# Optimization experiments

Measured on AMD Instinct MI355X. Metric: run time of the kernel, lower is better.

## Reference

```python
import jax, jax.numpy as jnp
import numpy as np

N = 20000            # nodes
E = 320000           # edges (before self loops)
NUM_PLAYERS = 5000
FEAT = 64            # feature_dim
H = 128              # hidden_dim
OUT = 10             # out_features
NEG_SLOPE = 0.2


def _p(key, shape, fan_in):
    return jax.random.normal(key, shape, dtype=jnp.float32) / np.sqrt(fan_in)


def setup_inputs() -> dict:
    key = jax.random.key(0)
    ks = jax.random.split(key, 20)
    # x_player: col 0 = player id (stored as float), cols 1: = features
    ids = jax.random.randint(ks[0], (N, 1), 0, NUM_PLAYERS + 1).astype(jnp.float32)
    feats = jax.random.normal(ks[1], (N, FEAT), dtype=jnp.float32)
    x_player = jnp.concatenate([ids, feats], axis=1)
    edge_index = jax.random.randint(ks[2], (2, E), 0, N, dtype=jnp.int32)
    return {
        "x_player": x_player,
        "edge_index": edge_index,
        "emb": jax.random.normal(ks[3], (NUM_PLAYERS + 1, H), dtype=jnp.float32),
        "proj_W": _p(ks[4], (H + FEAT, H), H + FEAT),
        "proj_b": jnp.zeros((H,), jnp.float32),
        "W1l": _p(ks[5], (H, 4 * H), H),
        "W1r": _p(ks[6], (H, 4 * H), H),
        "att1": _p(ks[7], (4, H), H),
        "b1": jnp.zeros((4 * H,), jnp.float32),
        "W2l": _p(ks[8], (4 * H, H), 4 * H),
        "W2r": _p(ks[9], (4 * H, H), 4 * H),
        "att2": _p(ks[10], (1, H), H),
        "b2": jnp.zeros((H,), jnp.float32),
        "out_W": _p(ks[11], (H, OUT), H),
        "out_b": jnp.zeros((OUT,), jnp.float32),
    }


def gatv2(x, src, dst, Wl, Wr, att, bias, heads, ch, concat):
    # GATv2Conv (PyG defaults: share_weights=False, negative_slope=0.2,
    # add_self_loops handled by caller, dropout off at eval)
    xl = (x @ Wl).reshape(N, heads, ch)   # source transform (x_j)
    xr = (x @ Wr).reshape(N, heads, ch)   # target transform (x_i)
    h = xl[src] + xr[dst]                                      # [E,H,C]
    e = jnp.sum(jax.nn.leaky_relu(h, NEG_SLOPE) * att, -1)     # [E,H]
    # segment softmax over incoming edges of each dst node
    m = jax.ops.segment_max(e, dst, num_segments=N)            # [N,H]
    ex = jnp.exp(e - m[dst])
    s = jax.ops.segment_sum(ex, dst, num_segments=N)
    alpha = ex / (s[dst] + 1e-16)                              # [E,H]
    out = jax.ops.segment_sum(alpha[..., None] * xl[src], dst, num_segments=N)
    out = out.reshape(N, heads * ch) if concat else out.mean(axis=1)
    return out + bias


def reference(x_player, edge_index, emb, proj_W, proj_b,
              W1l, W1r, att1, b1, W2l, W2r, att2, b2, out_W, out_b):
    ids = x_player[:, 0].astype(jnp.int32)
    combined = jnp.concatenate([emb[ids], x_player[:, 1:]], axis=1)
    x = jax.nn.relu(combined @ proj_W + proj_b)                # [N,H]
    # add self loops (GATv2Conv default)
    loop = jnp.arange(N, dtype=edge_index.dtype)
    src = jnp.concatenate([edge_index[0], loop])
    dst = jnp.concatenate([edge_index[1], loop])
    x = jax.nn.relu(gatv2(x, src, dst, W1l, W1r, att1, b1, 4, H, True))
    x = gatv2(x, src, dst, W2l, W2r, att2, b2, 1, H, True)
    return x @ out_W + out_b                                   # [N,OUT]
```

## Files before the change

kernel.cpp:

```cpp
#include <hip/hip_runtime.h>
#include <math.h>

#define NNODES 20000
#define XP_COLS 65

typedef unsigned int uint32;
typedef __attribute__((ext_vector_type(8))) short short8;
typedef __attribute__((ext_vector_type(4))) float float4v;

__device__ __forceinline__ float bflo(uint32 u){ return __uint_as_float(u << 16); }
__device__ __forceinline__ float bfhi(uint32 u){ return __uint_as_float(u & 0xffff0000u); }
__device__ __forceinline__ unsigned short f2bf(float f){
  uint32 u = __float_as_uint(f);
  uint32 r = (u + 0x7fffu + ((u >> 16) & 1u)) >> 16;
  return (unsigned short)r;
}
__device__ __forceinline__ void unpack8(uint4 u, float* x){
  x[0]=bflo(u.x); x[1]=bfhi(u.x); x[2]=bflo(u.y); x[3]=bfhi(u.y);
  x[4]=bflo(u.z); x[5]=bfhi(u.z); x[6]=bflo(u.w); x[7]=bfhi(u.w);
}

__global__ void k_count(const int* __restrict__ dst, int E, int* __restrict__ deg){
  int e = blockIdx.x * 256 + threadIdx.x;
  if (e < E) atomicAdd(&deg[dst[e]], 1);
}

__global__ __launch_bounds__(256) void k_scan(const int* __restrict__ deg,
                                              int* __restrict__ off,
                                              int* __restrict__ cursor){
  const int CH = 80;
  int tid = threadIdx.x;
  int lane = tid & 63, w = tid >> 6;
  int beg = tid * CH;
  bool act = beg < NNODES;
  int sum = 0;
  if (act){
    const int4* p = (const int4*)(deg + beg);
    #pragma unroll
    for (int i = 0; i < 20; i++){
      int4 v = p[i];
      sum += v.x + v.y + v.z + v.w + 4;
    }
  }
  int inc = sum;
  #pragma unroll
  for (int d = 1; d < 64; d <<= 1){
    int t = __shfl_up(inc, d, 64);
    if (lane >= d) inc += t;
  }
  __shared__ int wtot[4];
  if (lane == 63) wtot[w] = inc;
  __syncthreads();
  int wbase = 0;
  for (int i = 0; i < w; i++) wbase += wtot[i];
  int run = wbase + inc - sum;
  if (act){
    const int4* p = (const int4*)(deg + beg);
    int4* po = (int4*)(off + beg);
    int4* pc = (int4*)(cursor + beg);
    #pragma unroll
    for (int i = 0; i < 20; i++){
      int4 v = p[i];
      int4 o;
      o.x = run; run += v.x + 1;
      o.y = run; run += v.y + 1;
      o.z = run; run += v.z + 1;
      o.w = run; run += v.w + 1;
      po[i] = o; pc[i] = o;
    }
  }
  if (tid == 249) off[NNODES] = run;
}

__global__ void k_fill(const int* __restrict__ src, const int* __restrict__ dst, int E,
                       int* __restrict__ cursor, int* __restrict__ csr){
  int t = blockIdx.x * 256 + threadIdx.x;
  if (t < NNODES){
    int p = atomicAdd(&cursor[t], 1);
    csr[p] = t;
  } else if (t < NNODES + E){
    int e = t - NNODES;
    int p = atomicAdd(&cursor[dst[e]], 1);
    csr[p] = src[e];
  }
}

__global__ void k_cvt(const float* __restrict__ W1l, const float* __restrict__ W1r,
                      const float* __restrict__ W2l, const float* __restrict__ W2r,
                      const float* __restrict__ projW,
                      unsigned short* __restrict__ T1l, unsigned short* __restrict__ T1r,
                      unsigned short* __restrict__ T2l, unsigned short* __restrict__ T2r,
                      unsigned short* __restrict__ Tp){
  int idx = blockIdx.x * 256 + threadIdx.x;
  if (idx < 65536){
    int o = idx;
    int n = o >> 7, k = o & 127;
    T1l[o] = f2bf(W1l[k * 512 + n]);
  } else if (idx < 131072){
    int o = idx - 65536;
    int n = o >> 7, k = o & 127;
    T1r[o] = f2bf(W1r[k * 512 + n]);
  } else if (idx < 196608){
    int o = idx - 131072;
    int n = o >> 9, k = o & 511;
    T2l[o] = f2bf(W2l[k * 128 + n]);
  } else if (idx < 262144){
    int o = idx - 196608;
    int n = o >> 9, k = o & 511;
    T2r[o] = f2bf(W2r[k * 128 + n]);
  } else if (idx < 286720){
    int o = idx - 262144;
    int n = o / 192, k = o - n * 192;
    Tp[o] = f2bf(projW[k * 128 + n]);
  }
}

__global__ __launch_bounds__(256) void k_proj_mfma(const float* __restrict__ xp,
                                                   const float* __restrict__ emb,
                                                   const unsigned short* __restrict__ Bt,
                                                   const float* __restrict__ bias,
                                                   unsigned short* __restrict__ Xb){
  __shared__ unsigned short As[64][40];
  __shared__ unsigned short Bs[128][40];
  __shared__ int ids[64];
  int tid = threadIdx.x;
  int bm = blockIdx.x * 64;
  int w = tid >> 6, lane = tid & 63;
  int wm = (w >> 1) * 32, wn = (w & 1) * 64;
  int quad = lane >> 4, l16 = lane & 15;
  if (tid < 64){
    int g = bm + tid;
    ids[tid] = (g < NNODES) ? (int)xp[(size_t)g * XP_COLS] : 0;
  }
  float4v acc[2][4];
  #pragma unroll
  for (int i = 0; i < 2; i++)
    #pragma unroll
    for (int j = 0; j < 4; j++) acc[i][j] = (float4v){0.f,0.f,0.f,0.f};
  int am = tid >> 2, ak = (tid & 3) * 8;
  int gm = bm + am;
  bool mv = gm < NNODES;
  int brow = tid >> 1, bk = (tid & 1) * 16;
  __syncthreads();

  for (int k0 = 0; k0 < 192; k0 += 32){
    float v[8];
    if (k0 < 128){
      const float* ep = emb + (size_t)ids[am] * 128 + k0 + ak;
      float4 e0 = *(const float4*)ep;
      float4 e1 = *(const float4*)(ep + 4);
      v[0]=e0.x; v[1]=e0.y; v[2]=e0.z; v[3]=e0.w;
      v[4]=e1.x; v[5]=e1.y; v[6]=e1.z; v[7]=e1.w;
    } else {
      const float* fp = xp + (size_t)gm * XP_COLS + 1 + (k0 - 128) + ak;
      #pragma unroll
      for (int i = 0; i < 8; i++) v[i] = mv ? fp[i] : 0.f;
    }
    ushort4 o0, o1;
    o0.x=f2bf(v[0]); o0.y=f2bf(v[1]); o0.z=f2bf(v[2]); o0.w=f2bf(v[3]);
    o1.x=f2bf(v[4]); o1.y=f2bf(v[5]); o1.z=f2bf(v[6]); o1.w=f2bf(v[7]);
    *(ushort4*)&As[am][ak]     = o0;
    *(ushort4*)&As[am][ak + 4] = o1;
    const unsigned short* bp = Bt + (size_t)brow * 192 + k0 + bk;
    *(uint4*)&Bs[brow][bk]     = *(const uint4*)bp;
    *(uint4*)&Bs[brow][bk + 8] = *(const uint4*)(bp + 8);
    __syncthreads();
    short8 af[2], bf[4];
    #pragma unroll
    for (int t = 0; t < 2; t++) af[t] = *(const short8*)&As[wm + t * 16 + l16][quad * 8];
    #pragma unroll
    for (int t = 0; t < 4; t++) bf[t] = *(const short8*)&Bs[wn + t * 16 + l16][quad * 8];
    #pragma unroll
    for (int tm = 0; tm < 2; tm++)
      #pragma unroll
      for (int tn = 0; tn < 4; tn++)
        acc[tm][tn] = __builtin_amdgcn_mfma_f32_16x16x32_bf16(af[tm], bf[tn], acc[tm][tn], 0, 0, 0);
    __syncthreads();
  }
  #pragma unroll
  for (int tm = 0; tm < 2; tm++){
    #pragma unroll
    for (int r = 0; r < 4; r++){
      int row = bm + wm + tm * 16 + quad * 4 + r;
      if (row >= NNODES) continue;
      #pragma unroll
      for (int tn = 0; tn < 4; tn++){
        int col = wn + tn * 16 + l16;
        float val = fmaxf(acc[tm][tn][r] + bias[col], 0.f);
        Xb[(size_t)row * 128 + col] = f2bf(val);
      }
    }
  }
}

template<int K, int N, int MODE, int NH>
__global__ __launch_bounds__(256) void k_mfma(const unsigned short* __restrict__ A,
                                              const unsigned short* __restrict__ B0t,
                                              const unsigned short* __restrict__ B1t,
                                              void* __restrict__ C0, void* __restrict__ C1,
                                              const float* __restrict__ att,
                                              float* __restrict__ dl, float* __restrict__ dr){
  const unsigned short* Bt = blockIdx.z ? B1t : B0t;
  __shared__ unsigned short As[64][40];
  __shared__ unsigned short Bs[128][40];
  __shared__ float red[4][32];
  int tid = threadIdx.x;
  int bm = blockIdx.y * 64;
  int bn = blockIdx.x * 128;
  int head = (NH == 1) ? 0 : blockIdx.x;
  int w = tid >> 6, lane = tid & 63;
  int wm = (w >> 1) * 32, wn = (w & 1) * 64;
  int quad = lane >> 4, l16 = lane & 15;
  float av[4];
  #pragma unroll
  for (int tn = 0; tn < 4; tn++) av[tn] = att[head * 128 + wn + tn * 16 + l16];
  float4v acc[2][4];
  #pragma unroll
  for (int i = 0; i < 2; i++)
    #pragma unroll
    for (int j = 0; j < 4; j++) acc[i][j] = (float4v){0.f,0.f,0.f,0.f};
  int am = tid >> 2, ak = (tid & 3) * 8;
  int gm = bm + am;
  bool mv = gm < NNODES;
  int brow = tid >> 1, bk = (tid & 1) * 16;

  for (int k0 = 0; k0 < K; k0 += 32){
    uint4 va = {0u,0u,0u,0u};
    if (mv) va = *(const uint4*)(A + (size_t)gm * K + k0 + ak);
    *(uint4*)&As[am][ak] = va;
    const unsigned short* bp = Bt + (size_t)(bn + brow) * K + k0 + bk;
    *(uint4*)&Bs[brow][bk]     = *(const uint4*)bp;
    *(uint4*)&Bs[brow][bk + 8] = *(const uint4*)(bp + 8);
    __syncthreads();
    short8 af[2], bf[4];
    #pragma unroll
    for (int t = 0; t < 2; t++) af[t] = *(const short8*)&As[wm + t * 16 + l16][quad * 8];
    #pragma unroll
    for (int t = 0; t < 4; t++) bf[t] = *(const short8*)&Bs[wn + t * 16 + l16][quad * 8];
    #pragma unroll
    for (int tm = 0; tm < 2; tm++)
      #pragma unroll
      for (int tn = 0; tn < 4; tn++)
        acc[tm][tn] = __builtin_amdgcn_mfma_f32_16x16x32_bf16(af[tm], bf[tn], acc[tm][tn], 0, 0, 0);
    __syncthreads();
  }
  #pragma unroll
  for (int tm = 0; tm < 2; tm++){
    #pragma unroll
    for (int r = 0; r < 4; r++){
      int row = bm + wm + tm * 16 + quad * 4 + r;
      if (row < NNODES){
        #pragma unroll
        for (int tn = 0; tn < 4; tn++){
          int col = bn + wn + tn * 16 + l16;
          float val = acc[tm][tn][r];
          if (MODE == 0 || blockIdx.z == 0){
            unsigned short* C = (unsigned short*)(blockIdx.z ? C1 : C0);
            C[(size_t)row * N + col] = f2bf(val);
          } else {
            ((float*)C1)[(size_t)row * N + col] = val;
          }
        }
      }
      float pd = acc[tm][0][r] * av[0];
      pd = fmaf(acc[tm][1][r], av[1], pd);
      pd = fmaf(acc[tm][2][r], av[2], pd);
      pd = fmaf(acc[tm][3][r], av[3], pd);
      pd += __shfl_xor(pd, 1);
      pd += __shfl_xor(pd, 2);
      pd += __shfl_xor(pd, 4);
      pd += __shfl_xor(pd, 8);
      if (l16 == 0) red[w][tm * 16 + quad * 4 + r] = pd;
    }
  }
  __syncthreads();
  if (tid < 64){
    float v = (tid < 32) ? red[0][tid] + red[1][tid] : red[2][tid & 31] + red[3][tid & 31];
    int row = bm + tid;
    if (row < NNODES){
      float* D = blockIdx.z ? dr : dl;
      D[row * NH + head] = v;
    }
  }
}

__global__ __launch_bounds__(256) void k_attn1(const unsigned short* __restrict__ xl,
                                               const unsigned short* __restrict__ xr,
                                               const float* __restrict__ dl, const float* __restrict__ dr,
                                               const float* __restrict__ att, const float* __restrict__ bias,
                                               const int* __restrict__ off, const int* __restrict__ csr,
                                               unsigned short* __restrict__ out){
  int lane = threadIdx.x & 63;
  int n = blockIdx.x * 4 + (threadIdx.x >> 6);
  int h = lane >> 4;
  uint4 ur = *(const uint4*)(xr + (size_t)n * 512 + lane * 8);
  float r[8]; unpack8(ur, r);
  const float* ap = att + lane * 8;
  float4 A0 = *(const float4*)ap, A1 = *(const float4*)(ap + 4);
  float a[8] = {A0.x,A0.y,A0.z,A0.w,A1.x,A1.y,A1.z,A1.w};
  float c0 = 0.6f * dr[n * 4 + h];
  int beg = off[n], end = off[n + 1];

  float m = -INFINITY, s = 0.f;
  float acc[8] = {0,0,0,0,0,0,0,0};
  int j = beg;
  for (; j + 3 < end; j += 4){
    int sn0 = csr[j], sn1 = csr[j + 1], sn2 = csr[j + 2], sn3 = csr[j + 3];
    uint4 u0 = *(const uint4*)(xl + (size_t)sn0 * 512 + lane * 8);
    uint4 u1 = *(const uint4*)(xl + (size_t)sn1 * 512 + lane * 8);
    uint4 u2 = *(const uint4*)(xl + (size_t)sn2 * 512 + lane * 8);
    uint4 u3 = *(const uint4*)(xl + (size_t)sn3 * 512 + lane * 8);
    float d0 = dl[sn0 * 4 + h], d1 = dl[sn1 * 4 + h];
    float d2 = dl[sn2 * 4 + h], d3 = dl[sn3 * 4 + h];
    float x0[8], x1[8], x2[8], x3[8];
    unpack8(u0, x0); unpack8(u1, x1); unpack8(u2, x2); unpack8(u3, x3);
    float p0 = 0.f, p1 = 0.f, p2 = 0.f, p3 = 0.f;
    #pragma unroll
    for (int i = 0; i < 8; i++){
      p0 = fmaf(a[i], fabsf(x0[i] + r[i]), p0);
      p1 = fmaf(a[i], fabsf(x1[i] + r[i]), p1);
      p2 = fmaf(a[i], fabsf(x2[i] + r[i]), p2);
      p3 = fmaf(a[i], fabsf(x3[i] + r[i]), p3);
    }
    p0 += __shfl_xor(p0, 1); p1 += __shfl_xor(p1, 1); p2 += __shfl_xor(p2, 1); p3 += __shfl_xor(p3, 1);
    p0 += __shfl_xor(p0, 2); p1 += __shfl_xor(p1, 2); p2 += __shfl_xor(p2, 2); p3 += __shfl_xor(p3, 2);
    p0 += __shfl_xor(p0, 4); p1 += __shfl_xor(p1, 4); p2 += __shfl_xor(p2, 4); p3 += __shfl_xor(p3, 4);
    p0 += __shfl_xor(p0, 8); p1 += __shfl_xor(p1, 8); p2 += __shfl_xor(p2, 8); p3 += __shfl_xor(p3, 8);
    float e0 = fmaf(0.6f, d0, fmaf(0.4f, p0, c0));
    float e1 = fmaf(0.6f, d1, fmaf(0.4f, p1, c0));
    float e2 = fmaf(0.6f, d2, fmaf(0.4f, p2, c0));
    float e3 = fmaf(0.6f, d3, fmaf(0.4f, p3, c0));
    float emax = fmaxf(fmaxf(e0, e1), fmaxf(e2, e3));
    if (__any(emax > m)){
      float nm = fmaxf(m, emax);
      float al  = __expf(m - nm);
      float ex0 = __expf(e0 - nm), ex1 = __expf(e1 - nm);
      float ex2 = __expf(e2 - nm), ex3 = __expf(e3 - nm);
      m = nm;
      s = fmaf(s, al, (ex0 + ex1) + (ex2 + ex3));
      #pragma unroll
      for (int i = 0; i < 8; i++){
        float t = fmaf(ex0, x0[i], ex1 * x1[i]);
        t = fmaf(ex2, x2[i], t);
        t = fmaf(ex3, x3[i], t);
        acc[i] = fmaf(acc[i], al, t);
      }
    } else {
      float ex0 = __expf(e0 - m), ex1 = __expf(e1 - m);
      float ex2 = __expf(e2 - m), ex3 = __expf(e3 - m);
      s += (ex0 + ex1) + (ex2 + ex3);
      #pragma unroll
      for (int i = 0; i < 8; i++){
        float t = fmaf(ex0, x0[i], ex1 * x1[i]);
        t = fmaf(ex2, x2[i], t);
        acc[i] = fmaf(ex3, x3[i], acc[i] + t);
      }
    }
  }
  for (; j < end; j++){
    int sn = csr[j];
    float dls = dl[sn * 4 + h];
    uint4 ux = *(const uint4*)(xl + (size_t)sn * 512 + lane * 8);
    float x[8]; unpack8(ux, x);
    float p = 0.f;
    #pragma unroll
    for (int i = 0; i < 8; i++) p = fmaf(a[i], fabsf(x[i] + r[i]), p);
    p += __shfl_xor(p, 1);
    p += __shfl_xor(p, 2);
    p += __shfl_xor(p, 4);
    p += __shfl_xor(p, 8);
    float e = fmaf(0.6f, dls, fmaf(0.4f, p, c0));
    if (__any(e > m)){
      float nm = fmaxf(m, e);
      float al = __expf(m - nm);
      float ex = __expf(e - nm);
      m = nm;
      s = fmaf(s, al, ex);
      #pragma unroll
      for (int i = 0; i < 8; i++) acc[i] = fmaf(acc[i], al, ex * x[i]);
    } else {
      float ex = __expf(e - m);
      s += ex;
      #pragma unroll
      for (int i = 0; i < 8; i++) acc[i] = fmaf(ex, x[i], acc[i]);
    }
  }
  float inv = 1.f / (s + 1e-16f);
  const float* bp = bias + lane * 8;
  float4 B0 = *(const float4*)bp, B1 = *(const float4*)(bp + 4);
  float bb[8] = {B0.x,B0.y,B0.z,B0.w,B1.x,B1.y,B1.z,B1.w};
  unsigned short o[8];
  #pragma unroll
  for (int i = 0; i < 8; i++)
    o[i] = f2bf(fmaxf(fmaf(acc[i], inv, bb[i]), 0.f));
  uint4 ov;
  ov.x = (uint32)o[0] | ((uint32)o[1] << 16);
  ov.y = (uint32)o[2] | ((uint32)o[3] << 16);
  ov.z = (uint32)o[4] | ((uint32)o[5] << 16);
  ov.w = (uint32)o[6] | ((uint32)o[7] << 16);
  *(uint4*)(out + (size_t)n * 512 + lane * 8) = ov;
}

__global__ __launch_bounds__(256) void k_attn2(const unsigned short* __restrict__ xl,
                                               const float* __restrict__ xr,
                                               const float* __restrict__ dl, const float* __restrict__ dr,
                                               const float* __restrict__ att, const float* __restrict__ bias,
                                               const float* __restrict__ outW, const float* __restrict__ outb,
                                               const int* __restrict__ off, const int* __restrict__ csr,
                                               float* __restrict__ out){
  __shared__ float Wsh[1280];
  int tid = threadIdx.x;
  for (int i = tid; i < 1280; i += 256) Wsh[i] = outW[i];
  __syncthreads();
  int lane = tid & 63;
  int n = blockIdx.x * 4 + (tid >> 6);
  float2 rv = *(const float2*)(xr + (size_t)n * 128 + lane * 2);
  float2 av = *(const float2*)(att + lane * 2);
  float c0 = 0.6f * dr[n];
  int beg = off[n], end = off[n + 1];
  float m = -INFINITY, s = 0.f;
  float a0 = 0.f, a1 = 0.f;
  int j = beg;
  for (; j + 3 < end; j += 4){
    int sn0 = csr[j], sn1 = csr[j + 1], sn2 = csr[j + 2], sn3 = csr[j + 3];
    uint32 u0 = *(const uint32*)(xl + (size_t)sn0 * 128 + lane * 2);
    uint32 u1 = *(const uint32*)(xl + (size_t)sn1 * 128 + lane * 2);
    uint32 u2 = *(const uint32*)(xl + (size_t)sn2 * 128 + lane * 2);
    uint32 u3 = *(const uint32*)(xl + (size_t)sn3 * 128 + lane * 2);
    float d0 = dl[sn0], d1 = dl[sn1], d2 = dl[sn2], d3 = dl[sn3];
    float x00 = bflo(u0), x01 = bfhi(u0);
    float x10 = bflo(u1), x11 = bfhi(u1);
    float x20 = bflo(u2), x21 = bfhi(u2);
    float x30 = bflo(u3), x31 = bfhi(u3);
    float p0 = fmaf(av.x, fabsf(x00 + rv.x), av.y * fabsf(x01 + rv.y));
    float p1 = fmaf(av.x, fabsf(x10 + rv.x), av.y * fabsf(x11 + rv.y));
    float p2 = fmaf(av.x, fabsf(x20 + rv.x), av.y * fabsf(x21 + rv.y));
    float p3 = fmaf(av.x, fabsf(x30 + rv.x), av.y * fabsf(x31 + rv.y));
    p0 += __shfl_xor(p0, 1);  p1 += __shfl_xor(p1, 1);  p2 += __shfl_xor(p2, 1);  p3 += __shfl_xor(p3, 1);
    p0 += __shfl_xor(p0, 2);  p1 += __shfl_xor(p1, 2);  p2 += __shfl_xor(p2, 2);  p3 += __shfl_xor(p3, 2);
    p0 += __shfl_xor(p0, 4);  p1 += __shfl_xor(p1, 4);  p2 += __shfl_xor(p2, 4);  p3 += __shfl_xor(p3, 4);
    p0 += __shfl_xor(p0, 8);  p1 += __shfl_xor(p1, 8);  p2 += __shfl_xor(p2, 8);  p3 += __shfl_xor(p3, 8);
    p0 += __shfl_xor(p0, 16); p1 += __shfl_xor(p1, 16); p2 += __shfl_xor(p2, 16); p3 += __shfl_xor(p3, 16);
    p0 += __shfl_xor(p0, 32); p1 += __shfl_xor(p1, 32); p2 += __shfl_xor(p2, 32); p3 += __shfl_xor(p3, 32);
    float e0 = fmaf(0.6f, d0, fmaf(0.4f, p0, c0));
    float e1 = fmaf(0.6f, d1, fmaf(0.4f, p1, c0));
    float e2 = fmaf(0.6f, d2, fmaf(0.4f, p2, c0));
    float e3 = fmaf(0.6f, d3, fmaf(0.4f, p3, c0));
    float emax = fmaxf(fmaxf(e0, e1), fmaxf(e2, e3));
    if (emax > m){
      float al  = __expf(m - emax);
      float ex0 = __expf(e0 - emax), ex1 = __expf(e1 - emax);
      float ex2 = __expf(e2 - emax), ex3 = __expf(e3 - emax);
      m = emax;
      s  = fmaf(s,  al, (ex0 + ex1) + (ex2 + ex3));
      float t0 = fmaf(ex0, x00, ex1 * x10); t0 = fmaf(ex2, x20, t0); t0 = fmaf(ex3, x30, t0);
      float t1 = fmaf(ex0, x01, ex1 * x11); t1 = fmaf(ex2, x21, t1); t1 = fmaf(ex3, x31, t1);
      a0 = fmaf(a0, al, t0);
      a1 = fmaf(a1, al, t1);
    } else {
      float ex0 = __expf(e0 - m), ex1 = __expf(e1 - m);
      float ex2 = __expf(e2 - m), ex3 = __expf(e3 - m);
      s += (ex0 + ex1) + (ex2 + ex3);
      float t0 = fmaf(ex0, x00, ex1 * x10); t0 = fmaf(ex2, x20, t0);
      float t1 = fmaf(ex0, x01, ex1 * x11); t1 = fmaf(ex2, x21, t1);
      a0 = fmaf(ex3, x30, a0 + t0);
      a1 = fmaf(ex3, x31, a1 + t1);
    }
  }
  for (; j < end; j++){
    int sn = csr[j];
    float dls = dl[sn];
    uint32 u = *(const uint32*)(xl + (size_t)sn * 128 + lane * 2);
    float x0 = bflo(u), x1 = bfhi(u);
    float p = fmaf(av.x, fabsf(x0 + rv.x), av.y * fabsf(x1 + rv.y));
    p += __shfl_xor(p, 1);
    p += __shfl_xor(p, 2);
    p += __shfl_xor(p, 4);
    p += __shfl_xor(p, 8);
    p += __shfl_xor(p, 16);
    p += __shfl_xor(p, 32);
    float e = fmaf(0.6f, dls, fmaf(0.4f, p, c0));
    if (e > m){
      float al = __expf(m - e);
      m = e;
      s  = fmaf(s,  al, 1.f);
      a0 = fmaf(a0, al, x0);
      a1 = fmaf(a1, al, x1);
    } else {
      float ex = __expf(e - m);
      s += ex;
      a0 = fmaf(ex, x0, a0);
      a1 = fmaf(ex, x1, a1);
    }
  }
  float inv = 1.f / (s + 1e-16f);
  int c = lane * 2;
  float x2_0 = fmaf(a0, inv, bias[c]);
  float x2_1 = fmaf(a1, inv, bias[c + 1]);
  #pragma unroll
  for (int o = 0; o < 10; o++){
    float p = fmaf(x2_0, Wsh[c * 10 + o], x2_1 * Wsh[(c + 1) * 10 + o]);
    p += __shfl_xor(p, 1);
    p += __shfl_xor(p, 2);
    p += __shfl_xor(p, 4);
    p += __shfl_xor(p, 8);
    p += __shfl_xor(p, 16);
    p += __shfl_xor(p, 32);
    if (lane == 0) out[(size_t)n * 10 + o] = p + outb[o];
  }
}

extern "C" void kernel_launch(void* const* d_in, const int* in_sizes, int n_in,
                              void* d_out, int out_size, void* d_ws, size_t ws_size,
                              hipStream_t stream){
  const float* xp    = (const float*)d_in[0];
  const int*   ei    = (const int*)  d_in[1];
  const float* emb   = (const float*)d_in[2];
  const float* projW = (const float*)d_in[3];
  const float* projb = (const float*)d_in[4];
  const float* W1l   = (const float*)d_in[5];
  const float* W1r   = (const float*)d_in[6];
  const float* att1  = (const float*)d_in[7];
  const float* b1    = (const float*)d_in[8];
  const float* W2l   = (const float*)d_in[9];
  const float* W2r   = (const float*)d_in[10];
  const float* att2  = (const float*)d_in[11];
  const float* b2    = (const float*)d_in[12];
  const float* outW  = (const float*)d_in[13];
  const float* outb  = (const float*)d_in[14];
  float* out = (float*)d_out;

  int E = in_sizes[1] / 2;
  const int* esrc = ei;
  const int* edst = ei + E;

  char* w = (char*)d_ws;
  int* deg  = (int*)w; w += (size_t)NNODES * 4;
  int* off  = (int*)w; w += (size_t)(NNODES + 4) * 4;
  int* cur  = (int*)w; w += (size_t)NNODES * 4;
  int* csr  = (int*)w; w += (size_t)(NNODES + E) * 4;
  unsigned short* Xb   = (unsigned short*)w; w += (size_t)NNODES * 128 * 2;
  unsigned short* Wt1l = (unsigned short*)w; w += (size_t)512 * 128 * 2;
  unsigned short* Wt1r = (unsigned short*)w; w += (size_t)512 * 128 * 2;
  unsigned short* Wt2l = (unsigned short*)w; w += (size_t)128 * 512 * 2;
  unsigned short* Wt2r = (unsigned short*)w; w += (size_t)128 * 512 * 2;
  unsigned short* Wtp  = (unsigned short*)w; w += (size_t)128 * 192 * 2;
  unsigned short* xl1b = (unsigned short*)w; w += (size_t)NNODES * 512 * 2;
  unsigned short* xr1b = (unsigned short*)w; w += (size_t)NNODES * 512 * 2;
  unsigned short* X1b  = (unsigned short*)w; w += (size_t)NNODES * 512 * 2;
  unsigned short* xl2b = (unsigned short*)w; w += (size_t)NNODES * 128 * 2;
  float* xr2 = (float*)w; w += (size_t)NNODES * 128 * 4;
  float* dl1 = (float*)w; w += (size_t)NNODES * 4 * 4;
  float* dr1 = (float*)w; w += (size_t)NNODES * 4 * 4;
  float* dl2 = (float*)w; w += (size_t)NNODES * 4;
  float* dr2 = (float*)w; w += (size_t)NNODES * 4;

  hipMemsetAsync(deg, 0, (size_t)NNODES * 4, stream);
  k_count<<<(E + 255) / 256, 256, 0, stream>>>(edst, E, deg);
  k_scan<<<1, 256, 0, stream>>>(deg, off, cur);
  k_fill<<<(NNODES + E + 255) / 256, 256, 0, stream>>>(esrc, edst, E, cur, csr);

  k_cvt<<<1120, 256, 0, stream>>>(W1l, W1r, W2l, W2r, projW, Wt1l, Wt1r, Wt2l, Wt2r, Wtp);
  k_proj_mfma<<<dim3((NNODES + 63) / 64), 256, 0, stream>>>(xp, emb, Wtp, projb, Xb);
  k_mfma<128, 512, 0, 4><<<dim3(4, (NNODES + 63) / 64, 2), 256, 0, stream>>>(
      Xb, Wt1l, Wt1r, xl1b, xr1b, att1, dl1, dr1);
  k_attn1<<<NNODES / 4, 256, 0, stream>>>(xl1b, xr1b, dl1, dr1, att1, b1, off, csr, X1b);
  k_mfma<512, 128, 1, 1><<<dim3(1, (NNODES + 63) / 64, 2), 256, 0, stream>>>(
      X1b, Wt2l, Wt2r, xl2b, xr2, att2, dl2, dr2);
  k_attn2<<<NNODES / 4, 256, 0, stream>>>(xl2b, xr2, dl2, dr2, att2, b2, outW, outb, off, csr, out);
}
```

Before: 300.1 us.

## Replace online softmax max with precomputed global upper-bound shift

The GEMM epilogue also computes an absolute-value bound on each source's attention logit contribution and reduces it into a per-head global maximum with an integer atomicMax. Each destination combines that with its own |att|·|xr| term to form a fixed shift. The attention kernels can then drop online-softmax rescaling and branching, and gather 8 neighbours per iteration instead of 4. The degree-count kernel is also merged into the weight-conversion kernel, saving a launch. The loose bound risks exp underflow, and so accuracy loss, when actual logits sit far below it.

```diff
diff --git a/kernel.cpp b/kernel.cpp
--- a/kernel.cpp
+++ b/kernel.cpp
@@ -20,78 +20,19 @@
   x[4]=bflo(u.z); x[5]=bfhi(u.z); x[6]=bflo(u.w); x[7]=bfhi(u.w);
 }
 
-__global__ void k_count(const int* __restrict__ dst, int E, int* __restrict__ deg){
-  int e = blockIdx.x * 256 + threadIdx.x;
-  if (e < E) atomicAdd(&deg[dst[e]], 1);
-}
-
-__global__ __launch_bounds__(256) void k_scan(const int* __restrict__ deg,
-                                              int* __restrict__ off,
-                                              int* __restrict__ cursor){
-  const int CH = 80;
-  int tid = threadIdx.x;
-  int lane = tid & 63, w = tid >> 6;
-  int beg = tid * CH;
-  bool act = beg < NNODES;
-  int sum = 0;
-  if (act){
-    const int4* p = (const int4*)(deg + beg);
-    #pragma unroll
-    for (int i = 0; i < 20; i++){
-      int4 v = p[i];
-      sum += v.x + v.y + v.z + v.w + 4;
-    }
-  }
-  int inc = sum;
-  #pragma unroll
-  for (int d = 1; d < 64; d <<= 1){
-    int t = __shfl_up(inc, d, 64);
-    if (lane >= d) inc += t;
-  }
-  __shared__ int wtot[4];
-  if (lane == 63) wtot[w] = inc;
-  __syncthreads();
-  int wbase = 0;
-  for (int i = 0; i < w; i++) wbase += wtot[i];
-  int run = wbase + inc - sum;
-  if (act){
-    const int4* p = (const int4*)(deg + beg);
-    int4* po = (int4*)(off + beg);
-    int4* pc = (int4*)(cursor + beg);
-    #pragma unroll
-    for (int i = 0; i < 20; i++){
-      int4 v = p[i];
-      int4 o;
-      o.x = run; run += v.x + 1;
-      o.y = run; run += v.y + 1;
-      o.z = run; run += v.z + 1;
-      o.w = run; run += v.w + 1;
-      po[i] = o; pc[i] = o;
-    }
-  }
-  if (tid == 249) off[NNODES] = run;
-}
-
-__global__ void k_fill(const int* __restrict__ src, const int* __restrict__ dst, int E,
-                       int* __restrict__ cursor, int* __restrict__ csr){
-  int t = blockIdx.x * 256 + threadIdx.x;
-  if (t < NNODES){
-    int p = atomicAdd(&cursor[t], 1);
-    csr[p] = t;
-  } else if (t < NNODES + E){
-    int e = t - NNODES;
-    int p = atomicAdd(&cursor[dst[e]], 1);
-    csr[p] = src[e];
-  }
-}
-
-__global__ void k_cvt(const float* __restrict__ W1l, const float* __restrict__ W1r,
-                      const float* __restrict__ W2l, const float* __restrict__ W2r,
-                      const float* __restrict__ projW,
-                      unsigned short* __restrict__ T1l, unsigned short* __restrict__ T1r,
-                      unsigned short* __restrict__ T2l, unsigned short* __restrict__ T2r,
-                      unsigned short* __restrict__ Tp){
-  int idx = blockIdx.x * 256 + threadIdx.x;
+__global__ void k_cvt_count(const int* __restrict__ dst, int E, int* __restrict__ deg,
+                            const float* __restrict__ W1l, const float* __restrict__ W1r,
+                            const float* __restrict__ W2l, const float* __restrict__ W2r,
+                            const float* __restrict__ projW,
+                            unsigned short* __restrict__ T1l, unsigned short* __restrict__ T1r,
+                            unsigned short* __restrict__ T2l, unsigned short* __restrict__ T2r,
+                            unsigned short* __restrict__ Tp){
+  int gid = blockIdx.x * 256 + threadIdx.x;
+  if (gid < E){
+    atomicAdd(&deg[dst[gid]], 1);
+    return;
+  }
+  int idx = gid - E;
   if (idx < 65536){
     int o = idx;
     int n = o >> 7, k = o & 127;
@@ -115,6 +56,66 @@
   }
 }
 
+__global__ __launch_bounds__(256) void k_scan(const int* __restrict__ deg,
+                                              int* __restrict__ off,
+                                              int* __restrict__ cursor){
+  const int CH = 80;
+  int tid = threadIdx.x;
+  int lane = tid & 63, w = tid >> 6;
+  int beg = tid * CH;
+  bool act = beg < NNODES;
+  int sum = 0;
+  if (act){
+    const int4* p = (const int4*)(deg + beg);
+    #pragma unroll
+    for (int i = 0; i < 20; i++){
+      int4 v = p[i];
+      sum += v.x + v.y + v.z + v.w + 4;
+    }
+  }
+  int inc = sum;
+  #pragma unroll
+  for (int d = 1; d < 64; d <<= 1){
+    int t = __shfl_up(inc, d, 64);
+    if (lane >= d) inc += t;
+  }
+  __shared__ int wtot[4];
+  if (lane == 63) wtot[w] = inc;
+  __syncthreads();
+  int wbase = 0;
+  for (int i = 0; i < w; i++) wbase += wtot[i];
+  int run = wbase + inc - sum;
+  if (act){
+    const int4* p = (const int4*)(deg + beg);
+    int4* po = (int4*)(off + beg);
+    int4* pc = (int4*)(cursor + beg);
+    #pragma unroll
+    for (int i = 0; i < 20; i++){
+      int4 v = p[i];
+      int4 o;
+      o.x = run; run += v.x + 1;
+      o.y = run; run += v.y + 1;
+      o.z = run; run += v.z + 1;
+      o.w = run; run += v.w + 1;
+      po[i] = o; pc[i] = o;
+    }
+  }
+  if (tid == 249) off[NNODES] = run;
+}
+
+__global__ void k_fill(const int* __restrict__ src, const int* __restrict__ dst, int E,
+                       int* __restrict__ cursor, int* __restrict__ csr){
+  int t = blockIdx.x * 256 + threadIdx.x;
+  if (t < NNODES){
+    int p = atomicAdd(&cursor[t], 1);
+    csr[p] = t;
+  } else if (t < NNODES + E){
+    int e = t - NNODES;
+    int p = atomicAdd(&cursor[dst[e]], 1);
+    csr[p] = src[e];
+  }
+}
+
 __global__ __launch_bounds__(256) void k_proj_mfma(const float* __restrict__ xp,
                                                    const float* __restrict__ emb,
                                                    const unsigned short* __restrict__ Bt,
@@ -199,11 +200,13 @@
                                               const unsigned short* __restrict__ B1t,
                                               void* __restrict__ C0, void* __restrict__ C1,
                                               const float* __restrict__ att,
-                                              float* __restrict__ dl, float* __restrict__ dr){
+                                              float* __restrict__ dl, float* __restrict__ dr,
+                                              int* __restrict__ gmax){
   const unsigned short* Bt = blockIdx.z ? B1t : B0t;
   __shared__ unsigned short As[64][40];
   __shared__ unsigned short Bs[128][40];
   __shared__ float red[4][32];
+  __shared__ float redu[4][32];
   int tid = threadIdx.x;
   int bm = blockIdx.y * 64;
   int bn = blockIdx.x * 128;
@@ -211,9 +214,12 @@
   int w = tid >> 6, lane = tid & 63;
   int wm = (w >> 1) * 32, wn = (w & 1) * 64;
   int quad = lane >> 4, l16 = lane & 15;
-  float av[4];
-  #pragma unroll
-  for (int tn = 0; tn < 4; tn++) av[tn] = att[head * 128 + wn + tn * 16 + l16];
+  float av[4], aav[4];
+  #pragma unroll
+  for (int tn = 0; tn < 4; tn++){
+    av[tn] = att[head * 128 + wn + tn * 16 + l16];
+    aav[tn] = fabsf(av[tn]);
+  }
   float4v acc[2][4];
   #pragma unroll
   for (int i = 0; i < 2; i++)
@@ -266,20 +272,36 @@
       pd = fmaf(acc[tm][1][r], av[1], pd);
       pd = fmaf(acc[tm][2][r], av[2], pd);
       pd = fmaf(acc[tm][3][r], av[3], pd);
-      pd += __shfl_xor(pd, 1);
-      pd += __shfl_xor(pd, 2);
-      pd += __shfl_xor(pd, 4);
-      pd += __shfl_xor(pd, 8);
-      if (l16 == 0) red[w][tm * 16 + quad * 4 + r] = pd;
+      float pu = fabsf(acc[tm][0][r]) * aav[0];
+      pu = fmaf(fabsf(acc[tm][1][r]), aav[1], pu);
+      pu = fmaf(fabsf(acc[tm][2][r]), aav[2], pu);
+      pu = fmaf(fabsf(acc[tm][3][r]), aav[3], pu);
+      pd += __shfl_xor(pd, 1);  pu += __shfl_xor(pu, 1);
+      pd += __shfl_xor(pd, 2);  pu += __shfl_xor(pu, 2);
+      pd += __shfl_xor(pd, 4);  pu += __shfl_xor(pu, 4);
+      pd += __shfl_xor(pd, 8);  pu += __shfl_xor(pu, 8);
+      if (l16 == 0){
+        red[w][tm * 16 + quad * 4 + r]  = pd;
+        redu[w][tm * 16 + quad * 4 + r] = pu;
+      }
     }
   }
   __syncthreads();
   if (tid < 64){
-    float v = (tid < 32) ? red[0][tid] + red[1][tid] : red[2][tid & 31] + red[3][tid & 31];
+    float vd, vu;
+    if (tid < 32){ vd = red[0][tid] + red[1][tid];   vu = redu[0][tid] + redu[1][tid]; }
+    else { vd = red[2][tid & 31] + red[3][tid & 31]; vu = redu[2][tid & 31] + redu[3][tid & 31]; }
     int row = bm + tid;
-    if (row < NNODES){
+    bool ok = row < NNODES;
+    if (ok){
       float* D = blockIdx.z ? dr : dl;
-      D[row * NH + head] = v;
+      D[row * NH + head] = vd;
+    }
+    if (blockIdx.z == 0){
+      float v = ok ? fmaf(0.4f, vu, 0.6f * vd) : -4.0e6f;
+      #pragma unroll
+      for (int dd = 1; dd < 64; dd <<= 1) v = fmaxf(v, __shfl_xor(v, dd));
+      if (tid == 0) atomicMax(&gmax[head], (int)ceilf(v * 256.0f) + (1 << 30));
     }
   }
 }
@@ -288,6 +310,7 @@
                                                const unsigned short* __restrict__ xr,
                                                const float* __restrict__ dl, const float* __restrict__ dr,
                                                const float* __restrict__ att, const float* __restrict__ bias,
+                                               const int* __restrict__ gmax,
                                                const int* __restrict__ off, const int* __restrict__ csr,
                                                unsigned short* __restrict__ out){
   int lane = threadIdx.x & 63;
@@ -298,63 +321,54 @@
   const float* ap = att + lane * 8;
   float4 A0 = *(const float4*)ap, A1 = *(const float4*)(ap + 4);
   float a[8] = {A0.x,A0.y,A0.z,A0.w,A1.x,A1.y,A1.z,A1.w};
-  float c0 = 0.6f * dr[n * 4 + h];
+  float V = 0.f;
+  #pragma unroll
+  for (int i = 0; i < 8; i++) V = fmaf(fabsf(a[i]), fabsf(r[i]), V);
+  V += __shfl_xor(V, 1);
+  V += __shfl_xor(V, 2);
+  V += __shfl_xor(V, 4);
+  V += __shfl_xor(V, 8);
+  float Mg = (float)(gmax[h] - (1 << 30)) * (1.0f / 256.0f);
+  float base = fmaf(0.6f, dr[n * 4 + h], -Mg - 0.4f * V);
   int beg = off[n], end = off[n + 1];
 
-  float m = -INFINITY, s = 0.f;
+  float s = 0.f;
   float acc[8] = {0,0,0,0,0,0,0,0};
   int j = beg;
-  for (; j + 3 < end; j += 4){
-    int sn0 = csr[j], sn1 = csr[j + 1], sn2 = csr[j + 2], sn3 = csr[j + 3];
-    uint4 u0 = *(const uint4*)(xl + (size_t)sn0 * 512 + lane * 8);
-    uint4 u1 = *(const uint4*)(xl + (size_t)sn1 * 512 + lane * 8);
-    uint4 u2 = *(const uint4*)(xl + (size_t)sn2 * 512 + lane * 8);
-    uint4 u3 = *(const uint4*)(xl + (size_t)sn3 * 512 + lane * 8);
-    float d0 = dl[sn0 * 4 + h], d1 = dl[sn1 * 4 + h];
-    float d2 = dl[sn2 * 4 + h], d3 = dl[sn3 * 4 + h];
-    float x0[8], x1[8], x2[8], x3[8];
-    unpack8(u0, x0); unpack8(u1, x1); unpack8(u2, x2); unpack8(u3, x3);
-    float p0 = 0.f, p1 = 0.f, p2 = 0.f, p3 = 0.f;
-    #pragma unroll
-    for (int i = 0; i < 8; i++){
-      p0 = fmaf(a[i], fabsf(x0[i] + r[i]), p0);
-      p1 = fmaf(a[i], fabsf(x1[i] + r[i]), p1);
-      p2 = fmaf(a[i], fabsf(x2[i] + r[i]), p2);
-      p3 = fmaf(a[i], fabsf(x3[i] + r[i]), p3);
-    }
-    p0 += __shfl_xor(p0, 1); p1 += __shfl_xor(p1, 1); p2 += __shfl_xor(p2, 1); p3 += __shfl_xor(p3, 1);
-    p0 += __shfl_xor(p0, 2); p1 += __shfl_xor(p1, 2); p2 += __shfl_xor(p2, 2); p3 += __shfl_xor(p3, 2);
-    p0 += __shfl_xor(p0, 4); p1 += __shfl_xor(p1, 4); p2 += __shfl_xor(p2, 4); p3 += __shfl_xor(p3, 4);
-    p0 += __shfl_xor(p0, 8); p1 += __shfl_xor(p1, 8); p2 += __shfl_xor(p2, 8); p3 += __shfl_xor(p3, 8);
-    float e0 = fmaf(0.6f, d0, fmaf(0.4f, p0, c0));
-    float e1 = fmaf(0.6f, d1, fmaf(0.4f, p1, c0));
-    float e2 = fmaf(0.6f, d2, fmaf(0.4f, p2, c0));
-    float e3 = fmaf(0.6f, d3, fmaf(0.4f, p3, c0));
-    float emax = fmaxf(fmaxf(e0, e1), fmaxf(e2, e3));
-    if (__any(emax > m)){
-      float nm = fmaxf(m, emax);
-      float al  = __expf(m - nm);
-      float ex0 = __expf(e0 - nm), ex1 = __expf(e1 - nm);
-      float ex2 = __expf(e2 - nm), ex3 = __expf(e3 - nm);
-      m = nm;
-      s = fmaf(s, al, (ex0 + ex1) + (ex2 + ex3));
-      #pragma unroll
-      for (int i = 0; i < 8; i++){
-        float t = fmaf(ex0, x0[i], ex1 * x1[i]);
-        t = fmaf(ex2, x2[i], t);
-        t = fmaf(ex3, x3[i], t);
-        acc[i] = fmaf(acc[i], al, t);
+  for (; j + 7 < end; j += 8){
+    int sn[8]; uint4 u[8]; float d8[8];
+    #pragma unroll
+    for (int k = 0; k < 8; k++) sn[k] = csr[j + k];
+    #pragma unroll
+    for (int k = 0; k < 8; k++) u[k] = *(const uint4*)(xl + (size_t)sn[k] * 512 + lane * 8);
+    #pragma unroll
+    for (int k = 0; k < 8; k++) d8[k] = dl[sn[k] * 4 + h];
+    float p[8];
+    #pragma unroll
+    for (int k = 0; k < 8; k++){
+      float x[8]; unpack8(u[k], x);
+      float pa = 0.f, pb = 0.f;
+      #pragma unroll
+      for (int i = 0; i < 4; i++){
+        pa = fmaf(a[i],     fabsf(x[i]     + r[i]),     pa);
+        pb = fmaf(a[i + 4], fabsf(x[i + 4] + r[i + 4]), pb);
       }
-    } else {
-      float ex0 = __expf(e0 - m), ex1 = __expf(e1 - m);
-      float ex2 = __expf(e2 - m), ex3 = __expf(e3 - m);
-      s += (ex0 + ex1) + (ex2 + ex3);
-      #pragma unroll
-      for (int i = 0; i < 8; i++){
-        float t = fmaf(ex0, x0[i], ex1 * x1[i]);
-        t = fmaf(ex2, x2[i], t);
-        acc[i] = fmaf(ex3, x3[i], acc[i] + t);
-      }
+      p[k] = pa + pb;
+    }
+    #pragma unroll
+    for (int dd = 1; dd <= 8; dd <<= 1){
+      #pragma unroll
+      for (int k = 0; k < 8; k++) p[k] += __shfl_xor(p[k], dd);
+    }
+    float ex[8];
+    #pragma unroll
+    for (int k = 0; k < 8; k++) ex[k] = __expf(fmaf(0.4f, p[k], fmaf(0.6f, d8[k], base)));
+    s += ((ex[0] + ex[1]) + (ex[2] + ex[3])) + ((ex[4] + ex[5]) + (ex[6] + ex[7]));
+    #pragma unroll
+    for (int k = 0; k < 8; k++){
+      float x[8]; unpack8(u[k], x);
+      #pragma unroll
+      for (int i = 0; i < 8; i++) acc[i] = fmaf(ex[k], x[i], acc[i]);
     }
   }
   for (; j < end; j++){
@@ -362,28 +376,21 @@
     float dls = dl[sn * 4 + h];
     uint4 ux = *(const uint4*)(xl + (size_t)sn * 512 + lane * 8);
     float x[8]; unpack8(ux, x);
-    float p = 0.f;
-    #pragma unroll
-    for (int i = 0; i < 8; i++) p = fmaf(a[i], fabsf(x[i] + r[i]), p);
+    float pa = 0.f, pb = 0.f;
+    #pragma unroll
+    for (int i = 0; i < 4; i++){
+      pa = fmaf(a[i],     fabsf(x[i]     + r[i]),     pa);
+      pb = fmaf(a[i + 4], fabsf(x[i + 4] + r[i + 4]), pb);
+    }
+    float p = pa + pb;
     p += __shfl_xor(p, 1);
     p += __shfl_xor(p, 2);
     p += __shfl_xor(p, 4);
     p += __shfl_xor(p, 8);
-    float e = fmaf(0.6f, dls, fmaf(0.4f, p, c0));
-    if (__any(e > m)){
-      float nm = fmaxf(m, e);
-      float al = __expf(m - nm);
-      float ex = __expf(e - nm);
-      m = nm;
-      s = fmaf(s, al, ex);
-      #pragma unroll
-      for (int i = 0; i < 8; i++) acc[i] = fmaf(acc[i], al, ex * x[i]);
-    } else {
-      float ex = __expf(e - m);
-      s += ex;
-      #pragma unroll
-      for (int i = 0; i < 8; i++) acc[i] = fmaf(ex, x[i], acc[i]);
-    }
+    float ex = __expf(fmaf(0.4f, p, fmaf(0.6f, dls, base)));
+    s += ex;
+    #pragma unroll
+    for (int i = 0; i < 8; i++) acc[i] = fmaf(ex, x[i], acc[i]);
   }
   float inv = 1.f / (s + 1e-16f);
   const float* bp = bias + lane * 8;
@@ -406,6 +413,7 @@
                                                const float* __restrict__ dl, const float* __restrict__ dr,
                                                const float* __restrict__ att, const float* __restrict__ bias,
                                                const float* __restrict__ outW, const float* __restrict__ outb,
+                                               const int* __restrict__ gmax,
                                                const int* __restrict__ off, const int* __restrict__ csr,
                                                float* __restrict__ out){
   __shared__ float Wsh[1280];
@@ -416,55 +424,44 @@
   int n = blockIdx.x * 4 + (tid >> 6);
   float2 rv = *(const float2*)(xr + (size_t)n * 128 + lane * 2);
   float2 av = *(const float2*)(att + lane * 2);
-  float c0 = 0.6f * dr[n];
+  float V = fmaf(fabsf(av.x), fabsf(rv.x), fabsf(av.y) * fabsf(rv.y));
+  V += __shfl_xor(V, 1);
+  V += __shfl_xor(V, 2);
+  V += __shfl_xor(V, 4);
+  V += __shfl_xor(V, 8);
+  V += __shfl_xor(V, 16);
+  V += __shfl_xor(V, 32);
+  float Mg = (float)(gmax[0] - (1 << 30)) * (1.0f / 256.0f);
+  float base = fmaf(0.6f, dr[n], -Mg - 0.4f * V);
   int beg = off[n], end = off[n + 1];
-  float m = -INFINITY, s = 0.f;
+  float s = 0.f;
   float a0 = 0.f, a1 = 0.f;
   int j = beg;
-  for (; j + 3 < end; j += 4){
-    int sn0 = csr[j], sn1 = csr[j + 1], sn2 = csr[j + 2], sn3 = csr[j + 3];
-    uint32 u0 = *(const uint32*)(xl + (size_t)sn0 * 128 + lane * 2);
-    uint32 u1 = *(const uint32*)(xl + (size_t)sn1 * 128 + lane * 2);
-    uint32 u2 = *(const uint32*)(xl + (size_t)sn2 * 128 + lane * 2);
-    uint32 u3 = *(const uint32*)(xl + (size_t)sn3 * 128 + lane * 2);
-    float d0 = dl[sn0], d1 = dl[sn1], d2 = dl[sn2], d3 = dl[sn3];
-    float x00 = bflo(u0), x01 = bfhi(u0);
-    float x10 = bflo(u1), x11 = bfhi(u1);
-    float x20 = bflo(u2), x21 = bfhi(u2);
-    float x30 = bflo(u3), x31 = bfhi(u3);
-    float p0 = fmaf(av.x, fabsf(x00 + rv.x), av.y * fabsf(x01 + rv.y));
-    float p1 = fmaf(av.x, fabsf(x10 + rv.x), av.y * fabsf(x11 + rv.y));
-    float p2 = fmaf(av.x, fabsf(x20 + rv.x), av.y * fabsf(x21 + rv.y));
-    float p3 = fmaf(av.x, fabsf(x30 + rv.x), av.y * fabsf(x31 + rv.y));
-    p0 += __shfl_xor(p0, 1);  p1 += __shfl_xor(p1, 1);  p2 += __shfl_xor(p2, 1);  p3 += __shfl_xor(p3, 1);
-    p0 += __shfl_xor(p0, 2);  p1 += __shfl_xor(p1, 2);  p2 += __shfl_xor(p2, 2);  p3 += __shfl_xor(p3, 2);
-    p0 += __shfl_xor(p0, 4);  p1 += __shfl_xor(p1, 4);  p2 += __shfl_xor(p2, 4);  p3 += __shfl_xor(p3, 4);
-    p0 += __shfl_xor(p0, 8);  p1 += __shfl_xor(p1, 8);  p2 += __shfl_xor(p2, 8);  p3 += __shfl_xor(p3, 8);
-    p0 += __shfl_xor(p0, 16); p1 += __shfl_xor(p1, 16); p2 += __shfl_xor(p2, 16); p3 += __shfl_xor(p3, 16);
-    p0 += __shfl_xor(p0, 32); p1 += __shfl_xor(p1, 32); p2 += __shfl_xor(p2, 32); p3 += __shfl_xor(p3, 32);
-    float e0 = fmaf(0.6f, d0, fmaf(0.4f, p0, c0));
-    float e1 = fmaf(0.6f, d1, fmaf(0.4f, p1, c0));
-    float e2 = fmaf(0.6f, d2, fmaf(0.4f, p2, c0));
-    float e3 = fmaf(0.6f, d3, fmaf(0.4f, p3, c0));
-    float emax = fmaxf(fmaxf(e0, e1), fmaxf(e2, e3));
-    if (emax > m){
-      float al  = __expf(m - emax);
-      float ex0 = __expf(e0 - emax), ex1 = __expf(e1 - emax);
-      float ex2 = __expf(e2 - emax), ex3 = __expf(e3 - emax);
-      m = emax;
-      s  = fmaf(s,  al, (ex0 + ex1) + (ex2 + ex3));
-      float t0 = fmaf(ex0, x00, ex1 * x10); t0 = fmaf(ex2, x20, t0); t0 = fmaf(ex3, x30, t0);
-      float t1 = fmaf(ex0, x01, ex1 * x11); t1 = fmaf(ex2, x21, t1); t1 = fmaf(ex3, x31, t1);
-      a0 = fmaf(a0, al, t0);
-      a1 = fmaf(a1, al, t1);
-    } else {
-      float ex0 = __expf(e0 - m), ex1 = __expf(e1 - m);
-      float ex2 = __expf(e2 - m), ex3 = __expf(e3 - m);
-      s += (ex0 + ex1) + (ex2 + ex3);
-      float t0 = fmaf(ex0, x00, ex1 * x10); t0 = fmaf(ex2, x20, t0);
-      float t1 = fmaf(ex0, x01, ex1 * x11); t1 = fmaf(ex2, x21, t1);
-      a0 = fmaf(ex3, x30, a0 + t0);
-      a1 = fmaf(ex3, x31, a1 + t1);
+  for (; j + 7 < end; j += 8){
+    int sn[8]; uint32 u[8]; float d8[8];
+    #pragma unroll
+    for (int k = 0; k < 8; k++) sn[k] = csr[j + k];
+    #pragma unroll
+    for (int k = 0; k < 8; k++) u[k] = *(const uint32*)(xl + (size_t)sn[k] * 128 + lane * 2);
+    #pragma unroll
+    for (int k = 0; k < 8; k++) d8[k] = dl[sn[k]];
+    float p[8];
+    #pragma unroll
+    for (int k = 0; k < 8; k++)
+      p[k] = fmaf(av.x, fabsf(bflo(u[k]) + rv.x), av.y * fabsf(bfhi(u[k]) + rv.y));
+    #pragma unroll
+    for (int dd = 1; dd <= 32; dd <<= 1){
+      #pragma unroll
+      for (int k = 0; k < 8; k++) p[k] += __shfl_xor(p[k], dd);
+    }
+    float ex[8];
+    #pragma unroll
+    for (int k = 0; k < 8; k++) ex[k] = __expf(fmaf(0.4f, p[k], fmaf(0.6f, d8[k], base)));
+    s += ((ex[0] + ex[1]) + (ex[2] + ex[3])) + ((ex[4] + ex[5]) + (ex[6] + ex[7]));
+    #pragma unroll
+    for (int k = 0; k < 8; k++){
+      a0 = fmaf(ex[k], bflo(u[k]), a0);
+      a1 = fmaf(ex[k], bfhi(u[k]), a1);
     }
   }
   for (; j < end; j++){
@@ -479,19 +476,10 @@
     p += __shfl_xor(p, 8);
     p += __shfl_xor(p, 16);
     p += __shfl_xor(p, 32);
-    float e = fmaf(0.6f, dls, fmaf(0.4f, p, c0));
-    if (e > m){
-      float al = __expf(m - e);
-      m = e;
-      s  = fmaf(s,  al, 1.f);
-      a0 = fmaf(a0, al, x0);
-      a1 = fmaf(a1, al, x1);
-    } else {
-      float ex = __expf(e - m);
-      s += ex;
-      a0 = fmaf(ex, x0, a0);
-      a1 = fmaf(ex, x1, a1);
-    }
+    float ex = __expf(fmaf(0.4f, p, fmaf(0.6f, dls, base)));
+    s += ex;
+    a0 = fmaf(ex, x0, a0);
+    a1 = fmaf(ex, x1, a1);
   }
   float inv = 1.f / (s + 1e-16f);
   int c = lane * 2;
@@ -535,6 +523,7 @@
   const int* edst = ei + E;
 
   char* w = (char*)d_ws;
+  int* gmaxi = (int*)w; w += 32;
   int* deg  = (int*)w; w += (size_t)NNODES * 4;
   int* off  = (int*)w; w += (size_t)(NNODES + 4) * 4;
   int* cur  = (int*)w; w += (size_t)NNODES * 4;
@@ -555,17 +544,18 @@
   float* dl2 = (float*)w; w += (size_t)NNODES * 4;
   float* dr2 = (float*)w; w += (size_t)NNODES * 4;
 
-  hipMemsetAsync(deg, 0, (size_t)NNODES * 4, stream);
-  k_count<<<(E + 255) / 256, 256, 0, stream>>>(edst, E, deg);
+  hipMemsetAsync(gmaxi, 0, 32 + (size_t)NNODES * 4, stream);
+  int cvt_total = E + 286720;
+  k_cvt_count<<<(cvt_total + 255) / 256, 256, 0, stream>>>(
+      edst, E, deg, W1l, W1r, W2l, W2r, projW, Wt1l, Wt1r, Wt2l, Wt2r, Wtp);
   k_scan<<<1, 256, 0, stream>>>(deg, off, cur);
   k_fill<<<(NNODES + E + 255) / 256, 256, 0, stream>>>(esrc, edst, E, cur, csr);
 
-  k_cvt<<<1120, 256, 0, stream>>>(W1l, W1r, W2l, W2r, projW, Wt1l, Wt1r, Wt2l, Wt2r, Wtp);
   k_proj_mfma<<<dim3((NNODES + 63) / 64), 256, 0, stream>>>(xp, emb, Wtp, projb, Xb);
   k_mfma<128, 512, 0, 4><<<dim3(4, (NNODES + 63) / 64, 2), 256, 0, stream>>>(
-      Xb, Wt1l, Wt1r, xl1b, xr1b, att1, dl1, dr1);
-  k_attn1<<<NNODES / 4, 256, 0, stream>>>(xl1b, xr1b, dl1, dr1, att1, b1, off, csr, X1b);
+      Xb, Wt1l, Wt1r, xl1b, xr1b, att1, dl1, dr1, gmaxi);
+  k_attn1<<<NNODES / 4, 256, 0, stream>>>(xl1b, xr1b, dl1, dr1, att1, b1, gmaxi, off, csr, X1b);
   k_mfma<512, 128, 1, 1><<<dim3(1, (NNODES + 63) / 64, 2), 256, 0, stream>>>(
-      X1b, Wt2l, Wt2r, xl2b, xr2, att2, dl2, dr2);
-  k_attn2<<<NNODES / 4, 256, 0, stream>>>(xl2b, xr2, dl2, dr2, att2, b2, outW, outb, off, csr, out);
-}
+      X1b, Wt2l, Wt2r, xl2b, xr2, att2, dl2, dr2, gmaxi + 4);
+  k_attn2<<<NNODES / 4, 256, 0, stream>>>(xl2b, xr2, dl2, dr2, att2, b2, outW, outb, gmaxi + 4, off, csr, out);
+}
```

Result: slower. 323.2 us (+7.7%).
